# Optimization experiments

Hardware: AMD Instinct MI355X
Metric: run time of the kernel (lower is better)

## Reference

```python
import jax, jax.numpy as jnp
import numpy as np

B, S, DIM = 4, 2048, 1024
HEADS, HD = 16, DIM // 16
HIDDEN, LEVELS = 4 * DIM, 3
LN_EPS = 1e-5


def setup_inputs() -> dict:
    key = jax.random.key(0)
    ks = jax.random.split(key, 10)
    w = lambda k, shape: (jax.random.normal(k, shape, jnp.float32) * 0.02)
    return {
        "x": jax.random.normal(ks[0], (B, S, DIM), jnp.float32),
        "Wq": w(ks[1], (DIM, DIM)),
        "Wk": w(ks[2], (DIM, DIM)),
        "Wv": w(ks[3], (DIM, DIM)),
        "Wo": w(ks[4], (DIM, DIM)),
        "ln1_g": jnp.ones((DIM,), jnp.float32),
        "ln1_b": jnp.zeros((DIM,), jnp.float32),
        "ln2_g": jnp.ones((DIM,), jnp.float32),
        "ln2_b": jnp.zeros((DIM,), jnp.float32),
        "cms_w1": w(ks[5], (LEVELS, DIM, HIDDEN)),
        "cms_b1": jnp.zeros((LEVELS, HIDDEN), jnp.float32),
        "cms_w2": w(ks[6], (LEVELS, HIDDEN, DIM)),
        "cms_b2": jnp.zeros((LEVELS, DIM), jnp.float32),
    }


def _layer_norm(x, g, b):
    m = jnp.mean(x, axis=-1, keepdims=True)
    v = jnp.var(x, axis=-1, keepdims=True)
    return (x - m) * jax.lax.rsqrt(v + LN_EPS) * g + b


def _linear_attn(h, Wq, Wk, Wv, Wo):
    # h: [B, S, DIM]; feature_map(z) = elu(z) + 1 applied to Q and K
    fm = lambda z: jax.nn.elu(z) + 1.0
    Q = fm(h @ Wq).reshape(B, S, HEADS, HD)
    K = fm(h @ Wk).reshape(B, S, HEADS, HD)
    V = (h @ Wv).reshape(B, S, HEADS, HD)
    # scan over time with fast-weight memory M_t = M_{t-1} + k_t (x) v_t
    Qs = jnp.moveaxis(Q, 1, 0)  # [S, B, H, D]
    Ks = jnp.moveaxis(K, 1, 0)
    Vs = jnp.moveaxis(V, 1, 0)

    def step(carry, qkv):
        mem, ksum = carry  # [B,H,D,D], [B,H,D]
        q, k, v = qkv      # each [B,H,D]
        mem = mem + k[..., :, None] * v[..., None, :]
        ksum = ksum + k
        num = jnp.einsum('bhde,bhd->bhe', mem, q)
        den = jnp.einsum('bhd,bhd->bh', ksum, q)[..., None] + 1e-6
        return (mem, ksum), num / den

    init = (jnp.zeros((B, HEADS, HD, HD), h.dtype),
            jnp.zeros((B, HEADS, HD), h.dtype))
    _, ys = jax.lax.scan(step, init, (Qs, Ks, Vs))  # ys: [S,B,H,D]
    out = jnp.moveaxis(ys, 0, 1).reshape(B, S, DIM)
    return out @ Wo


def _cms(h, w1, b1, w2, b2):
    # Continuum Memory System: chain of LEVELS MLPs (dim->4dim->dim).
    y = h
    for l in range(LEVELS):
        y = jax.nn.gelu(y @ w1[l] + b1[l]) @ w2[l] + b2[l]
    return y


def reference(x, Wq, Wk, Wv, Wo, ln1_g, ln1_b, ln2_g, ln2_b,
              cms_w1, cms_b1, cms_w2, cms_b2):
    x = x + _linear_attn(_layer_norm(x, ln1_g, ln1_b), Wq, Wk, Wv, Wo)
    x = x + _cms(_layer_norm(x, ln2_g, ln2_b), cms_w1, cms_b1, cms_w2, cms_b2)
    return x
```

## Files before the change

### kernel.cpp

```cpp
#include <hip/hip_runtime.h>
#include <stdint.h>
#include <math.h>

#define DIM     1024
#define HID     4096
#define SEQ     2048
#define NB      4
#define NH      16
#define HD      64
#define NCHUNK  32
#define MROWS   8192

typedef unsigned short ushort_t;
typedef __attribute__((ext_vector_type(8))) short bf16x8;
typedef __attribute__((ext_vector_type(4))) float f32x4;

#define OFF_H    ((size_t)0)
#define OFF_Q    ((size_t)16777216)
#define OFF_K    ((size_t)33554432)
#define OFF_V    ((size_t)50331648)
#define OFF_P    ((size_t)67108864)
#define OFF_KS   ((size_t)100663296)
#define OFF_X1   ((size_t)101187584)
#define OFF_WQT  ((size_t)134742016)
#define OFF_WKT  ((size_t)136839168)
#define OFF_WVT  ((size_t)138936320)
#define OFF_WOT  ((size_t)141033472)
#define OFF_W1T  ((size_t)143130624)
#define OFF_W2T  ((size_t)168296448)
#define OFF_HIDB OFF_K

__device__ __forceinline__ float b2f(ushort_t u) {
    return __uint_as_float(((unsigned int)u) << 16);
}
__device__ __forceinline__ ushort_t f2b(float f) {
    unsigned int u = __float_as_uint(f);
    u += 0x7FFFu + ((u >> 16) & 1u);
    return (ushort_t)(u >> 16);
}
__device__ __forceinline__ void unpack4(uint2 u, float* f) {
    f[0] = __uint_as_float(u.x << 16);
    f[1] = __uint_as_float(u.x & 0xffff0000u);
    f[2] = __uint_as_float(u.y << 16);
    f[3] = __uint_as_float(u.y & 0xffff0000u);
}
__device__ __forceinline__ void ldg16(const ushort_t* g, ushort_t* l) {
    __builtin_amdgcn_global_load_lds(
        (const __attribute__((address_space(1))) void*)g,
        (__attribute__((address_space(3))) void*)l, 16, 0, 0);
}

__global__ void __launch_bounds__(256)
transpose_f32_bf16(const float* __restrict__ src, ushort_t* __restrict__ dst, int R, int C)
{
    __shared__ float t[32][33];
    const int bx = blockIdx.x * 32;
    const int by = blockIdx.y * 32;
    const int tx = threadIdx.x, ty = threadIdx.y;
    #pragma unroll
    for (int i = ty; i < 32; i += 8)
        t[i][tx] = src[(size_t)(by + i) * C + bx + tx];
    __syncthreads();
    #pragma unroll
    for (int i = ty; i < 32; i += 8)
        dst[(size_t)(bx + i) * R + by + tx] = f2b(t[tx][i]);
}

__global__ void __launch_bounds__(256)
ln_fwd(const float* __restrict__ xin, const float* __restrict__ g,
       const float* __restrict__ be, ushort_t* __restrict__ out)
{
    const int row = blockIdx.x, tid = threadIdx.x;
    const float4 f = ((const float4*)(xin + (size_t)row * DIM))[tid];
    float v[4] = {f.x, f.y, f.z, f.w};
    float s  = v[0] + v[1] + v[2] + v[3];
    float ss = v[0]*v[0] + v[1]*v[1] + v[2]*v[2] + v[3]*v[3];
    #pragma unroll
    for (int off = 32; off; off >>= 1) {
        s  += __shfl_down(s, off);
        ss += __shfl_down(ss, off);
    }
    __shared__ float red[2][4];
    const int wave = tid >> 6, lane = tid & 63;
    if (lane == 0) { red[0][wave] = s; red[1][wave] = ss; }
    __syncthreads();
    s  = red[0][0] + red[0][1] + red[0][2] + red[0][3];
    ss = red[1][0] + red[1][1] + red[1][2] + red[1][3];
    const float mean = s * (1.0f / DIM);
    const float var  = ss * (1.0f / DIM) - mean * mean;
    const float rstd = rsqrtf(var + 1e-5f);
    ushort_t o[4];
    #pragma unroll
    for (int i = 0; i < 4; i++) {
        const int col = tid * 4 + i;
        o[i] = f2b((v[i] - mean) * rstd * g[col] + be[col]);
    }
    uint2 u2;
    u2.x = (unsigned int)o[0] | ((unsigned int)o[1] << 16);
    u2.y = (unsigned int)o[2] | ((unsigned int)o[3] << 16);
    *(uint2*)(out + (size_t)row * DIM + tid * 4) = u2;
}

#define ACT_NONE 0
#define ACT_ELU1 1
#define ACT_GELU 2

template<int ACT, bool BIAS, bool RES, bool OUTF32>
__global__ void __launch_bounds__(256)
gemm_bt(const ushort_t* __restrict__ A, const ushort_t* __restrict__ Bt,
        const float* __restrict__ bias, const float* __restrict__ resid,
        void* __restrict__ Cout, int M, int N, int K)
{
    __shared__ __align__(16) ushort_t As[128 * 32];
    __shared__ __align__(16) ushort_t Bs[128 * 32];
    const int tid  = threadIdx.x;
    const int wave = tid >> 6, lane = tid & 63;
    const int bm = blockIdx.x * 128, bn = blockIdx.y * 128;
    const int wm = (wave >> 1) * 64, wn = (wave & 1) * 64;
    const int srow = tid >> 2;
    const int skp  = (tid & 3) * 8;
    const int mrow = lane & 15, kq = (lane >> 4) * 8;

    f32x4 acc[4][4] = {};

    const size_t arow0 = (size_t)(bm + srow)      * K;
    const size_t arow1 = (size_t)(bm + srow + 64) * K;
    const size_t brow0 = (size_t)(bn + srow)      * K;
    const size_t brow1 = (size_t)(bn + srow + 64) * K;

    for (int kt = 0; kt < K; kt += 32) {
        __syncthreads();
        ldg16(A  + arow0 + kt + skp, As + tid * 8);
        ldg16(A  + arow1 + kt + skp, As + 2048 + tid * 8);
        ldg16(Bt + brow0 + kt + skp, Bs + tid * 8);
        ldg16(Bt + brow1 + kt + skp, Bs + 2048 + tid * 8);
        __syncthreads();
        bf16x8 af[4], bfr[4];
        #pragma unroll
        for (int r = 0; r < 4; r++)
            af[r] = *(const bf16x8*)(As + (wm + r * 16 + mrow) * 32 + kq);
        #pragma unroll
        for (int c = 0; c < 4; c++)
            bfr[c] = *(const bf16x8*)(Bs + (wn + c * 16 + mrow) * 32 + kq);
        #pragma unroll
        for (int r = 0; r < 4; r++)
            #pragma unroll
            for (int c = 0; c < 4; c++)
                acc[r][c] = __builtin_amdgcn_mfma_f32_16x16x32_bf16(af[r], bfr[c], acc[r][c], 0, 0, 0);
    }

    const int cr = (lane >> 4) * 4;
    const int cc = lane & 15;
    #pragma unroll
    for (int r = 0; r < 4; r++) {
        #pragma unroll
        for (int c = 0; c < 4; c++) {
            const int gc = bn + wn + c * 16 + cc;
            const float bv = BIAS ? bias[gc] : 0.0f;
            #pragma unroll
            for (int j = 0; j < 4; j++) {
                const int gr = bm + wm + r * 16 + cr + j;
                float vv = acc[r][c][j] + bv;
                if (ACT == ACT_ELU1) vv = (vv > 0.0f) ? (vv + 1.0f) : expf(vv);
                if (ACT == ACT_GELU) {
                    const float x3 = vv * vv * vv;
                    vv = 0.5f * vv * (1.0f + tanhf(0.7978845608028654f * (vv + 0.044715f * x3)));
                }
                const size_t oidx = (size_t)gr * N + gc;
                if (RES) vv += resid[oidx];
                if (OUTF32) ((float*)Cout)[oidx] = vv;
                else        ((ushort_t*)Cout)[oidx] = f2b(vv);
            }
        }
    }
}

__global__ void __launch_bounds__(256)
attn_phase1(const ushort_t* __restrict__ K_, const ushort_t* __restrict__ V_,
            float* __restrict__ P, float* __restrict__ Ksum)
{
    const int c = blockIdx.x, h = blockIdx.y, b = blockIdx.z;
    __shared__ ushort_t Ks[64][68], Vs[64][68];
    const int tid = threadIdx.x;
    const size_t rowbase = (size_t)b * SEQ + c * 64;
    #pragma unroll
    for (int i = 0; i < 4; i++) {
        const int lin = tid + 256 * i;
        const int t = lin >> 4, d4 = (lin & 15) * 4;
        const size_t gidx = (rowbase + t) * DIM + h * HD + d4;
        *(uint2*)&Ks[t][d4] = *(const uint2*)(K_ + gidx);
        *(uint2*)&Vs[t][d4] = *(const uint2*)(V_ + gidx);
    }
    __syncthreads();
    const int d0 = (tid >> 4) * 4, e0 = (tid & 15) * 4;
    float acc[4][4] = {};
    for (int t = 0; t < 64; t++) {
        float kf[4], vf[4];
        unpack4(*(const uint2*)&Ks[t][d0], kf);
        unpack4(*(const uint2*)&Vs[t][e0], vf);
        #pragma unroll
        for (int i = 0; i < 4; i++)
            #pragma unroll
            for (int j = 0; j < 4; j++)
                acc[i][j] += kf[i] * vf[j];
    }
    const size_t pbase = (((size_t)b * NH + h) * NCHUNK + c) * 4096;
    #pragma unroll
    for (int i = 0; i < 4; i++) {
        float4 o; o.x = acc[i][0]; o.y = acc[i][1]; o.z = acc[i][2]; o.w = acc[i][3];
        *(float4*)(P + pbase + (size_t)(d0 + i) * 64 + e0) = o;
    }
    if (tid < 64) {
        float a = 0.0f;
        for (int t = 0; t < 64; t++) a += b2f(Ks[t][tid]);
        Ksum[(((size_t)b * NH + h) * NCHUNK + c) * 64 + tid] = a;
    }
}

__global__ void __launch_bounds__(256)
attn_prefix(float* __restrict__ P, float* __restrict__ Ksum)
{
    const int bh = blockIdx.y;
    const int e  = blockIdx.x * 256 + threadIdx.x;
    const size_t base = (size_t)bh * NCHUNK * 4096 + e;
    float acc = 0.0f;
    #pragma unroll
    for (int c = 0; c < NCHUNK; c++) {
        const float t = P[base + (size_t)c * 4096];
        P[base + (size_t)c * 4096] = acc;
        acc += t;
    }
    if (blockIdx.x == 0 && threadIdx.x < 64) {
        const size_t kb = (size_t)bh * NCHUNK * 64 + threadIdx.x;
        float a = 0.0f;
        #pragma unroll
        for (int c = 0; c < NCHUNK; c++) {
            const float t = Ksum[kb + c * 64];
            Ksum[kb + c * 64] = a;
            a += t;
        }
    }
}

__global__ void __launch_bounds__(256)
attn_phase2(const ushort_t* Q_, const ushort_t* __restrict__ K_,
            const ushort_t* __restrict__ V_, const float* __restrict__ P,
            const float* __restrict__ Ksum, ushort_t* Out)
{
    const int c = blockIdx.x, h = blockIdx.y, b = blockIdx.z;
    const int tid = threadIdx.x;
    __shared__ ushort_t Qs[64][68], KsB[64][68], VsB[64][68];
    __shared__ float S[64][68];
    __shared__ float Mp[64][64];
    __shared__ float kp[64];
    __shared__ float partial[4][64];
    const size_t rowbase = (size_t)b * SEQ + c * 64;
    const size_t pbase = (((size_t)b * NH + h) * NCHUNK + c) * 4096;
    #pragma unroll
    for (int i = 0; i < 4; i++) {
        const int lin = tid + 256 * i;
        const int t = lin >> 4, d4 = (lin & 15) * 4;
        const size_t gidx = (rowbase + t) * DIM + h * HD + d4;
        *(uint2*)&Qs[t][d4]  = *(const uint2*)(Q_ + gidx);
        *(uint2*)&KsB[t][d4] = *(const uint2*)(K_ + gidx);
        *(uint2*)&VsB[t][d4] = *(const uint2*)(V_ + gidx);
        *(float4*)&Mp[t][d4] = *(const float4*)(P + pbase + lin * 4);
    }
    if (tid < 64) kp[tid] = Ksum[(((size_t)b * NH + h) * NCHUNK + c) * 64 + tid];
    __syncthreads();

    const int t0 = (tid >> 4) * 4;
    const int c0 = (tid & 15) * 4;

    {
        float accS[4][4] = {};
        for (int d4 = 0; d4 < 64; d4 += 4) {
            float qf[4][4], kf[4][4];
            #pragma unroll
            for (int i = 0; i < 4; i++) {
                unpack4(*(const uint2*)&Qs[t0 + i][d4], qf[i]);
                unpack4(*(const uint2*)&KsB[c0 + i][d4], kf[i]);
            }
            #pragma unroll
            for (int i = 0; i < 4; i++)
                #pragma unroll
                for (int j = 0; j < 4; j++)
                    #pragma unroll
                    for (int dd = 0; dd < 4; dd++)
                        accS[i][j] += qf[i][dd] * kf[j][dd];
        }
        #pragma unroll
        for (int i = 0; i < 4; i++) {
            float4 sv;
            sv.x = (c0 + 0 <= t0 + i) ? accS[i][0] : 0.0f;
            sv.y = (c0 + 1 <= t0 + i) ? accS[i][1] : 0.0f;
            sv.z = (c0 + 2 <= t0 + i) ? accS[i][2] : 0.0f;
            sv.w = (c0 + 3 <= t0 + i) ? accS[i][3] : 0.0f;
            *(float4*)&S[t0 + i][c0] = sv;
        }
    }
    __syncthreads();

    {
        const int t = tid & 63, q = tid >> 6;
        const int base = q * 16;
        float a = 0.0f;
        #pragma unroll
        for (int ii = 0; ii < 16; ii++) a += S[t][base + ii];
        #pragma unroll
        for (int d = 0; d < 16; d++) a += b2f(Qs[t][base + d]) * kp[base + d];
        partial[q][t] = a;
    }
    __syncthreads();

    float acc[4][4] = {};
    for (int ii = 0; ii < 64; ii++) {
        float vf[4];
        unpack4(*(const uint2*)&VsB[ii][c0], vf);
        #pragma unroll
        for (int i = 0; i < 4; i++) {
            const float s = S[t0 + i][ii];
            #pragma unroll
            for (int j = 0; j < 4; j++) acc[i][j] += s * vf[j];
        }
    }
    for (int d = 0; d < 64; d++) {
        const float4 mp = *(const float4*)&Mp[d][c0];
        #pragma unroll
        for (int i = 0; i < 4; i++) {
            const float qv = b2f(Qs[t0 + i][d]);
            acc[i][0] += qv * mp.x; acc[i][1] += qv * mp.y;
            acc[i][2] += qv * mp.z; acc[i][3] += qv * mp.w;
        }
    }
    #pragma unroll
    for (int i = 0; i < 4; i++) {
        const float dent = partial[0][t0 + i] + partial[1][t0 + i] +
                           partial[2][t0 + i] + partial[3][t0 + i] + 1e-6f;
        const float r = 1.0f / dent;
        ushort_t o[4];
        #pragma unroll
        for (int j = 0; j < 4; j++) o[j] = f2b(acc[i][j] * r);
        uint2 u2;
        u2.x = (unsigned int)o[0] | ((unsigned int)o[1] << 16);
        u2.y = (unsigned int)o[2] | ((unsigned int)o[3] << 16);
        *(uint2*)(Out + (rowbase + t0 + i) * DIM + h * HD + c0) = u2;
    }
}

extern "C" void kernel_launch(void* const* d_in, const int* in_sizes, int n_in,
                              void* d_out, int out_size, void* d_ws, size_t ws_size,
                              hipStream_t stream)
{
    const float* x      = (const float*)d_in[0];
    const float* Wq     = (const float*)d_in[1];
    const float* Wk     = (const float*)d_in[2];
    const float* Wv     = (const float*)d_in[3];
    const float* Wo     = (const float*)d_in[4];
    const float* ln1g   = (const float*)d_in[5];
    const float* ln1b   = (const float*)d_in[6];
    const float* ln2g   = (const float*)d_in[7];
    const float* ln2b   = (const float*)d_in[8];
    const float* cw1    = (const float*)d_in[9];
    const float* cb1    = (const float*)d_in[10];
    const float* cw2    = (const float*)d_in[11];
    const float* cb2    = (const float*)d_in[12];

    char* ws = (char*)d_ws;
    ushort_t* h    = (ushort_t*)(ws + OFF_H);
    ushort_t* qb   = (ushort_t*)(ws + OFF_Q);
    ushort_t* kb   = (ushort_t*)(ws + OFF_K);
    ushort_t* vb   = (ushort_t*)(ws + OFF_V);
    float*    Pb   = (float*)(ws + OFF_P);
    float*    ksb  = (float*)(ws + OFF_KS);
    float*    x1   = (float*)(ws + OFF_X1);
    ushort_t* wqt  = (ushort_t*)(ws + OFF_WQT);
    ushort_t* wkt  = (ushort_t*)(ws + OFF_WKT);
    ushort_t* wvt  = (ushort_t*)(ws + OFF_WVT);
    ushort_t* wot  = (ushort_t*)(ws + OFF_WOT);
    ushort_t* w1t  = (ushort_t*)(ws + OFF_W1T);
    ushort_t* w2t  = (ushort_t*)(ws + OFF_W2T);
    ushort_t* hid  = (ushort_t*)(ws + OFF_HIDB);
    float*    outp = (float*)d_out;

    const dim3 tb(32, 8);
    transpose_f32_bf16<<<dim3(32, 32), tb, 0, stream>>>(Wq, wqt, DIM, DIM);
    transpose_f32_bf16<<<dim3(32, 32), tb, 0, stream>>>(Wk, wkt, DIM, DIM);
    transpose_f32_bf16<<<dim3(32, 32), tb, 0, stream>>>(Wv, wvt, DIM, DIM);
    transpose_f32_bf16<<<dim3(32, 32), tb, 0, stream>>>(Wo, wot, DIM, DIM);
    for (int l = 0; l < 3; l++) {
        transpose_f32_bf16<<<dim3(128, 32), tb, 0, stream>>>(cw1 + (size_t)l * DIM * HID,
                                                             w1t + (size_t)l * HID * DIM, DIM, HID);
        transpose_f32_bf16<<<dim3(32, 128), tb, 0, stream>>>(cw2 + (size_t)l * HID * DIM,
                                                             w2t + (size_t)l * DIM * HID, HID, DIM);
    }

    ln_fwd<<<MROWS, 256, 0, stream>>>(x, ln1g, ln1b, h);

    gemm_bt<ACT_ELU1, false, false, false><<<dim3(64, 8), 256, 0, stream>>>(h, wqt, nullptr, nullptr, qb, MROWS, DIM, DIM);
    gemm_bt<ACT_ELU1, false, false, false><<<dim3(64, 8), 256, 0, stream>>>(h, wkt, nullptr, nullptr, kb, MROWS, DIM, DIM);
    gemm_bt<ACT_NONE, false, false, false><<<dim3(64, 8), 256, 0, stream>>>(h, wvt, nullptr, nullptr, vb, MROWS, DIM, DIM);

    attn_phase1<<<dim3(NCHUNK, NH, NB), 256, 0, stream>>>(kb, vb, Pb, ksb);
    attn_prefix<<<dim3(16, 64), 256, 0, stream>>>(Pb, ksb);
    attn_phase2<<<dim3(NCHUNK, NH, NB), 256, 0, stream>>>(qb, kb, vb, Pb, ksb, qb);

    gemm_bt<ACT_NONE, false, true, true><<<dim3(64, 8), 256, 0, stream>>>(qb, wot, nullptr, x, x1, MROWS, DIM, DIM);

    ln_fwd<<<MROWS, 256, 0, stream>>>(x1, ln2g, ln2b, h);

    const ushort_t* cur = h;
    for (int l = 0; l < 3; l++) {
        gemm_bt<ACT_GELU, true, false, false><<<dim3(64, 32), 256, 0, stream>>>(
            cur, w1t + (size_t)l * HID * DIM, cb1 + (size_t)l * HID, nullptr, hid, MROWS, HID, DIM);
        if (l < 2) {
            gemm_bt<ACT_NONE, true, false, false><<<dim3(64, 8), 256, 0, stream>>>(
                hid, w2t + (size_t)l * DIM * HID, cb2 + (size_t)l * DIM, nullptr, h, MROWS, DIM, HID);
            cur = h;
        } else {
            gemm_bt<ACT_NONE, true, true, true><<<dim3(64, 8), 256, 0, stream>>>(
                hid, w2t + (size_t)l * DIM * HID, cb2 + (size_t)l * DIM, x1, outp, MROWS, DIM, HID);
        }
    }
    (void)in_sizes; (void)n_in; (void)out_size; (void)ws_size;
}
```

Baseline: 1.048 ms.

## Fuse Q/K/V projections into one GEMM and use fast GELU/ELU epilogues

The three separate Q, K and V projection GEMMs become one GEMM over a concatenated transposed weight of width 3072. The epilogue applies ELU+1 only to the Q and K column ranges, and the attention kernels read from the interleaved QKV buffer with stride 3072. The tanh-based GELU and expf-based ELU are also replaced with exp2/rcp formulations, which changes numerics slightly. The attention output now goes to the h buffer, and the hidden buffer is relocated within the workspace.

```diff
diff --git a/kernel.cpp b/kernel.cpp
--- a/kernel.cpp
+++ b/kernel.cpp
@@ -10,6 +10,7 @@
 #define HD      64
 #define NCHUNK  32
 #define MROWS   8192
+#define QSTR    3072
 
 typedef unsigned short ushort_t;
 typedef __attribute__((ext_vector_type(8))) short bf16x8;
@@ -17,18 +18,14 @@
 
 #define OFF_H    ((size_t)0)
 #define OFF_Q    ((size_t)16777216)
-#define OFF_K    ((size_t)33554432)
-#define OFF_V    ((size_t)50331648)
 #define OFF_P    ((size_t)67108864)
 #define OFF_KS   ((size_t)100663296)
 #define OFF_X1   ((size_t)101187584)
 #define OFF_WQT  ((size_t)134742016)
-#define OFF_WKT  ((size_t)136839168)
-#define OFF_WVT  ((size_t)138936320)
 #define OFF_WOT  ((size_t)141033472)
 #define OFF_W1T  ((size_t)143130624)
 #define OFF_W2T  ((size_t)168296448)
-#define OFF_HIDB OFF_K
+#define OFF_HIDB OFF_Q + 16777216
 
 __device__ __forceinline__ float b2f(ushort_t u) {
     return __uint_as_float(((unsigned int)u) << 16);
@@ -43,6 +40,14 @@
     f[1] = __uint_as_float(u.x & 0xffff0000u);
     f[2] = __uint_as_float(u.y << 16);
     f[3] = __uint_as_float(u.y & 0xffff0000u);
+}
+__device__ __forceinline__ float fast_gelu(float x) {
+    const float u = x * (1.5957691216057308f + 0.07135481627f * x * x);
+    const float e = exp2f(-1.4426950408889634f * u);
+    return x * __builtin_amdgcn_rcpf(1.0f + e);
+}
+__device__ __forceinline__ float fast_elu1(float x) {
+    return x > 0.0f ? x + 1.0f : exp2f(1.4426950408889634f * x);
 }
 __device__ __forceinline__ void ldg16(const ushort_t* g, ushort_t* l) {
     __builtin_amdgcn_global_load_lds(
@@ -104,6 +109,7 @@
 #define ACT_NONE 0
 #define ACT_ELU1 1
 #define ACT_GELU 2
+#define ACT_QKV  3
 
 template<int ACT, bool BIAS, bool RES, bool OUTF32>
 __global__ void __launch_bounds__(256)
@@ -120,6 +126,7 @@
     const int srow = tid >> 2;
     const int skp  = (tid & 3) * 8;
     const int mrow = lane & 15, kq = (lane >> 4) * 8;
+    const bool qkv_elu = (bn < 2048);
 
     f32x4 acc[4][4] = {};
 
@@ -161,11 +168,9 @@
             for (int j = 0; j < 4; j++) {
                 const int gr = bm + wm + r * 16 + cr + j;
                 float vv = acc[r][c][j] + bv;
-                if (ACT == ACT_ELU1) vv = (vv > 0.0f) ? (vv + 1.0f) : expf(vv);
-                if (ACT == ACT_GELU) {
-                    const float x3 = vv * vv * vv;
-                    vv = 0.5f * vv * (1.0f + tanhf(0.7978845608028654f * (vv + 0.044715f * x3)));
-                }
+                if (ACT == ACT_ELU1) vv = fast_elu1(vv);
+                if (ACT == ACT_GELU) vv = fast_gelu(vv);
+                if (ACT == ACT_QKV)  vv = qkv_elu ? fast_elu1(vv) : vv;
                 const size_t oidx = (size_t)gr * N + gc;
                 if (RES) vv += resid[oidx];
                 if (OUTF32) ((float*)Cout)[oidx] = vv;
@@ -176,7 +181,7 @@
 }
 
 __global__ void __launch_bounds__(256)
-attn_phase1(const ushort_t* __restrict__ K_, const ushort_t* __restrict__ V_,
+attn_phase1(const ushort_t* __restrict__ qkv,
             float* __restrict__ P, float* __restrict__ Ksum)
 {
     const int c = blockIdx.x, h = blockIdx.y, b = blockIdx.z;
@@ -187,9 +192,9 @@
     for (int i = 0; i < 4; i++) {
         const int lin = tid + 256 * i;
         const int t = lin >> 4, d4 = (lin & 15) * 4;
-        const size_t gidx = (rowbase + t) * DIM + h * HD + d4;
-        *(uint2*)&Ks[t][d4] = *(const uint2*)(K_ + gidx);
-        *(uint2*)&Vs[t][d4] = *(const uint2*)(V_ + gidx);
+        const size_t gidx = (rowbase + t) * QSTR + h * HD + d4;
+        *(uint2*)&Ks[t][d4] = *(const uint2*)(qkv + 1024 + gidx);
+        *(uint2*)&Vs[t][d4] = *(const uint2*)(qkv + 2048 + gidx);
     }
     __syncthreads();
     const int d0 = (tid >> 4) * 4, e0 = (tid & 15) * 4;
@@ -243,9 +248,8 @@
 }
 
 __global__ void __launch_bounds__(256)
-attn_phase2(const ushort_t* Q_, const ushort_t* __restrict__ K_,
-            const ushort_t* __restrict__ V_, const float* __restrict__ P,
-            const float* __restrict__ Ksum, ushort_t* Out)
+attn_phase2(const ushort_t* __restrict__ qkv, const float* __restrict__ P,
+            const float* __restrict__ Ksum, ushort_t* __restrict__ Out)
 {
     const int c = blockIdx.x, h = blockIdx.y, b = blockIdx.z;
     const int tid = threadIdx.x;
@@ -260,10 +264,10 @@
     for (int i = 0; i < 4; i++) {
         const int lin = tid + 256 * i;
         const int t = lin >> 4, d4 = (lin & 15) * 4;
-        const size_t gidx = (rowbase + t) * DIM + h * HD + d4;
-        *(uint2*)&Qs[t][d4]  = *(const uint2*)(Q_ + gidx);
-        *(uint2*)&KsB[t][d4] = *(const uint2*)(K_ + gidx);
-        *(uint2*)&VsB[t][d4] = *(const uint2*)(V_ + gidx);
+        const size_t gidx = (rowbase + t) * QSTR + h * HD + d4;
+        *(uint2*)&Qs[t][d4]  = *(const uint2*)(qkv + gidx);
+        *(uint2*)&KsB[t][d4] = *(const uint2*)(qkv + 1024 + gidx);
+        *(uint2*)&VsB[t][d4] = *(const uint2*)(qkv + 2048 + gidx);
         *(float4*)&Mp[t][d4] = *(const float4*)(P + pbase + lin * 4);
     }
     if (tid < 64) kp[tid] = Ksum[(((size_t)b * NH + h) * NCHUNK + c) * 64 + tid];
@@ -367,26 +371,22 @@
     const float* cb2    = (const float*)d_in[12];
 
     char* ws = (char*)d_ws;
-    ushort_t* h    = (ushort_t*)(ws + OFF_H);
-    ushort_t* qb   = (ushort_t*)(ws + OFF_Q);
-    ushort_t* kb   = (ushort_t*)(ws + OFF_K);
-    ushort_t* vb   = (ushort_t*)(ws + OFF_V);
-    float*    Pb   = (float*)(ws + OFF_P);
-    float*    ksb  = (float*)(ws + OFF_KS);
-    float*    x1   = (float*)(ws + OFF_X1);
-    ushort_t* wqt  = (ushort_t*)(ws + OFF_WQT);
-    ushort_t* wkt  = (ushort_t*)(ws + OFF_WKT);
-    ushort_t* wvt  = (ushort_t*)(ws + OFF_WVT);
-    ushort_t* wot  = (ushort_t*)(ws + OFF_WOT);
-    ushort_t* w1t  = (ushort_t*)(ws + OFF_W1T);
-    ushort_t* w2t  = (ushort_t*)(ws + OFF_W2T);
-    ushort_t* hid  = (ushort_t*)(ws + OFF_HIDB);
-    float*    outp = (float*)d_out;
+    ushort_t* h     = (ushort_t*)(ws + OFF_H);
+    ushort_t* qkv   = (ushort_t*)(ws + OFF_Q);
+    float*    Pb    = (float*)(ws + OFF_P);
+    float*    ksb   = (float*)(ws + OFF_KS);
+    float*    x1    = (float*)(ws + OFF_X1);
+    ushort_t* wqkvt = (ushort_t*)(ws + OFF_WQT);
+    ushort_t* wot   = (ushort_t*)(ws + OFF_WOT);
+    ushort_t* w1t   = (ushort_t*)(ws + OFF_W1T);
+    ushort_t* w2t   = (ushort_t*)(ws + OFF_W2T);
+    ushort_t* hid   = (ushort_t*)(ws + OFF_HIDB);
+    float*    outp  = (float*)d_out;
 
     const dim3 tb(32, 8);
-    transpose_f32_bf16<<<dim3(32, 32), tb, 0, stream>>>(Wq, wqt, DIM, DIM);
-    transpose_f32_bf16<<<dim3(32, 32), tb, 0, stream>>>(Wk, wkt, DIM, DIM);
-    transpose_f32_bf16<<<dim3(32, 32), tb, 0, stream>>>(Wv, wvt, DIM, DIM);
+    transpose_f32_bf16<<<dim3(32, 32), tb, 0, stream>>>(Wq, wqkvt,                   DIM, DIM);
+    transpose_f32_bf16<<<dim3(32, 32), tb, 0, stream>>>(Wk, wqkvt + 1024 * 1024,     DIM, DIM);
+    transpose_f32_bf16<<<dim3(32, 32), tb, 0, stream>>>(Wv, wqkvt + 2 * 1024 * 1024, DIM, DIM);
     transpose_f32_bf16<<<dim3(32, 32), tb, 0, stream>>>(Wo, wot, DIM, DIM);
     for (int l = 0; l < 3; l++) {
         transpose_f32_bf16<<<dim3(128, 32), tb, 0, stream>>>(cw1 + (size_t)l * DIM * HID,
@@ -397,15 +397,14 @@
 
     ln_fwd<<<MROWS, 256, 0, stream>>>(x, ln1g, ln1b, h);
 
-    gemm_bt<ACT_ELU1, false, false, false><<<dim3(64, 8), 256, 0, stream>>>(h, wqt, nullptr, nullptr, qb, MROWS, DIM, DIM);
-    gemm_bt<ACT_ELU1, false, false, false><<<dim3(64, 8), 256, 0, stream>>>(h, wkt, nullptr, nullptr, kb, MROWS, DIM, DIM);
-    gemm_bt<ACT_NONE, false, false, false><<<dim3(64, 8), 256, 0, stream>>>(h, wvt, nullptr, nullptr, vb, MROWS, DIM, DIM);
-
-    attn_phase1<<<dim3(NCHUNK, NH, NB), 256, 0, stream>>>(kb, vb, Pb, ksb);
+    gemm_bt<ACT_QKV, false, false, false><<<dim3(64, 24), 256, 0, stream>>>(
+        h, wqkvt, nullptr, nullptr, qkv, MROWS, QSTR, DIM);
+
+    attn_phase1<<<dim3(NCHUNK, NH, NB), 256, 0, stream>>>(qkv, Pb, ksb);
     attn_prefix<<<dim3(16, 64), 256, 0, stream>>>(Pb, ksb);
-    attn_phase2<<<dim3(NCHUNK, NH, NB), 256, 0, stream>>>(qb, kb, vb, Pb, ksb, qb);
-
-    gemm_bt<ACT_NONE, false, true, true><<<dim3(64, 8), 256, 0, stream>>>(qb, wot, nullptr, x, x1, MROWS, DIM, DIM);
+    attn_phase2<<<dim3(NCHUNK, NH, NB), 256, 0, stream>>>(qkv, Pb, ksb, h);
+
+    gemm_bt<ACT_NONE, false, true, true><<<dim3(64, 8), 256, 0, stream>>>(h, wot, nullptr, x, x1, MROWS, DIM, DIM);
 
     ln_fwd<<<MROWS, 256, 0, stream>>>(x1, ln2g, ln2b, h);
 
```

Result: no change. 1.047 ms (-0.0%).
